# Optimization experiments

Measured on AMD Instinct MI355X. Metric: run time of the kernel, lower is better.

The kernel has to match this reference:

```python
import jax, jax.numpy as jnp
import numpy as np

# Dimensions
T = 1024      # tokens
D = 1024      # d_model
DFF = 1024    # expert intermediate dim
R = 64        # tucker rank (r_in == r_out)
G = 8         # n_group
E = 32        # experts_per_group
NEXP = G * E  # 256 routed experts
K = 8         # top-k


def setup_inputs() -> dict:
    key = jax.random.key(0)
    ks = jax.random.split(key, 12)
    s = 0.02
    return {
        "x": jax.random.normal(ks[0], (T, D), jnp.float32),
        "Wg": jax.random.normal(ks[1], (D, NEXP), jnp.float32) * s,
        "uin_gate": jax.random.normal(ks[2], (G, D, R), jnp.float32) * s,
        "core_gate": jax.random.normal(ks[3], (G, E, R, R), jnp.float32) * s,
        "uout_gate": jax.random.normal(ks[4], (G, R, DFF), jnp.float32) * s,
        "uin_up": jax.random.normal(ks[5], (G, D, R), jnp.float32) * s,
        "core_up": jax.random.normal(ks[6], (G, E, R, R), jnp.float32) * s,
        "uout_up": jax.random.normal(ks[7], (G, R, DFF), jnp.float32) * s,
        "uin_down": jax.random.normal(ks[8], (G, DFF, R), jnp.float32) * s,
        "core_down": jax.random.normal(ks[9], (G, E, R, R), jnp.float32) * s,
        "uout_down": jax.random.normal(ks[10], (G, R, D), jnp.float32) * s,
    }


def _moe_forward(x, Wg, uin_gate, core_gate, uout_gate,
                 uin_up, core_up, uout_up,
                 uin_down, core_down, uout_down):
    Tn, d = x.shape
    # Router: top-k over 256 experts, softmax over the k logits (fp32 as in torch)
    logits = x @ Wg                                   # [T, NEXP]
    w, sel = jax.lax.top_k(logits, K)                 # [T, K]
    w = jax.nn.softmax(w.astype(jnp.float32), axis=-1).astype(x.dtype)

    e = sel.reshape(-1)                               # [F] global expert id
    g = e // E                                        # [F] group id
    tok = jnp.repeat(jnp.arange(Tn), K)               # [F] source token id
    mask = (g[:, None] == jnp.arange(G)[None, :]).astype(x.dtype)  # [F, G]

    def gather_in(uin):
        # project tokens with every group's u_in once, then gather per pair
        pre = jnp.einsum('td,gdr->gtr', x, uin)       # [G, T, R]
        return pre[g, tok]                            # [F, R]

    def core_apply(xin, core):
        # per-pair Tucker core slice bmm: x.unsqueeze(1) @ core[rel_idx]
        slices = core.reshape(G * E, R, R)[e]         # [F, R, R] gather
        return jnp.einsum('fr,fro->fo', xin, slices)  # [F, R]

    def group_out(h, U):
        # per-pair group-specific projection: h[f] @ U[g_f]
        out = jnp.zeros((h.shape[0], U.shape[-1]), h.dtype)
        for gi in range(G):  # fixed small loop over 8 groups
            out = out + (h * mask[:, gi:gi + 1]) @ U[gi]
        return out

    gate_h = group_out(core_apply(gather_in(uin_gate), core_gate), uout_gate)  # [F, DFF]
    up_h = group_out(core_apply(gather_in(uin_up), core_up), uout_up)          # [F, DFF]
    act = jax.nn.silu(gate_h) * up_h                                           # SwiGLU
    xin_d = group_out(act, uin_down)                                           # [F, R]
    out_f = group_out(core_apply(xin_d, core_down), uout_down)                 # [F, D]
    out_f = out_f * w.reshape(-1)[:, None]
    # scatter-add expert outputs back to tokens
    return jax.ops.segment_sum(out_f, tok, num_segments=Tn)


def reference(x, Wg, uin_gate, core_gate, uout_gate,
              uin_up, core_up, uout_up,
              uin_down, core_down, uout_down):
    return _moe_forward(x, Wg, uin_gate, core_gate, uout_gate,
                        uin_up, core_up, uout_up,
                        uin_down, core_down, uout_down)
```

## Files before the change

kernel.cpp:

```cpp
#include <hip/hip_runtime.h>
#include <hip/hip_bf16.h>
#include <math.h>


#define T_ 1024
#define D_ 1024
#define DFF_ 1024
#define R_ 64
#define G_ 8
#define E_ 32
#define NEXP_ 256
#define K_ 8
#define F_ 8192
#define LKZ_ 4
#define LTB_ 8
#define PKZ_ 2
#define DKZ_ 4
#define LP_ 72

typedef short bf16x8 __attribute__((ext_vector_type(8)));
typedef float f32x4 __attribute__((ext_vector_type(4)));

__device__ __forceinline__ unsigned short f2bf(float f) {
  unsigned int u = __float_as_uint(f);
  u += 0x7fffu + ((u >> 16) & 1u);
  return (unsigned short)(u >> 16);
}

__device__ __forceinline__ void stage_tile(short* dst, const unsigned short* src,
                                           int gp, int tid) {
  for (int idx = tid; idx < 512; idx += 256) {
    int r = idx >> 3, c8 = (idx & 7) << 3;
    *(uint4*)&dst[r * LP_ + c8] = *(const uint4*)&src[(size_t)r * gp + c8];
  }
}

__device__ __forceinline__ void stage_tile_guard(short* dst, const unsigned short* src,
                                                 int gp, int rows_valid, int tid) {
  for (int idx = tid; idx < 512; idx += 256) {
    int r = idx >> 3, c8 = (idx & 7) << 3;
    uint4 v = make_uint4(0u, 0u, 0u, 0u);
    if (r < rows_valid) v = *(const uint4*)&src[(size_t)r * gp + c8];
    *(uint4*)&dst[r * LP_ + c8] = v;
  }
}

__device__ __forceinline__ void stage_tile_f32(short* dst, const float* src,
                                               int gp, int tid) {
  for (int idx = tid; idx < 512; idx += 256) {
    int r = idx >> 3, c8 = (idx & 7) << 3;
    const float* s = &src[(size_t)r * gp + c8];
    float4 v0 = *(const float4*)s;
    float4 v1 = *(const float4*)(s + 4);
    uint4 u;
    u.x = ((unsigned)f2bf(v0.y) << 16) | f2bf(v0.x);
    u.y = ((unsigned)f2bf(v0.w) << 16) | f2bf(v0.z);
    u.z = ((unsigned)f2bf(v1.y) << 16) | f2bf(v1.x);
    u.w = ((unsigned)f2bf(v1.w) << 16) | f2bf(v1.z);
    *(uint4*)&dst[r * LP_ + c8] = u;
  }
}

__device__ __forceinline__ void mma_strip(const short* As, const short* Bs,
                                          int ms, int lane, f32x4* acc) {
  int lm = lane & 15;
  int lk = (lane >> 4) << 3;
#pragma unroll
  for (int kc = 0; kc < 64; kc += 32) {
    bf16x8 a = *(const bf16x8*)&As[(ms + lm) * LP_ + kc + lk];
#pragma unroll
    for (int nt = 0; nt < 4; ++nt) {
      bf16x8 b = *(const bf16x8*)&Bs[(nt * 16 + lm) * LP_ + kc + lk];
      acc[nt] = __builtin_amdgcn_mfma_f32_16x16x32_bf16(a, b, acc[nt], 0, 0, 0);
    }
  }
}

__global__ __launch_bounds__(256) void k_prep_logits(
    const float* __restrict__ x, const float* __restrict__ Wg,
    const float* __restrict__ s0, const float* __restrict__ s1,
    const float* __restrict__ s2, const float* __restrict__ s3,
    const float* __restrict__ s4, const float* __restrict__ s5,
    unsigned short* __restrict__ xb,
    unsigned short* __restrict__ d0, unsigned short* __restrict__ d1,
    unsigned short* __restrict__ d2, unsigned short* __restrict__ d3,
    unsigned short* __restrict__ d4, unsigned short* __restrict__ d5,
    int* __restrict__ cnt, float* __restrict__ Yf, float* __restrict__ lp) {
  __shared__ float shbuf[64 * 65];
  int b = blockIdx.x;
  if (b < 896) {
    int id = b >> 7, rem = b & 127, g = rem >> 4, tile = rem & 15;
    if (id == 6) {
      size_t base = ((size_t)g * 16 + tile) * 8192;
      for (int i = threadIdx.x; i < 2048; i += 256) {
        size_t idx = base + (size_t)i * 4;
        float4 v = *(const float4*)&x[idx];
        xb[idx + 0] = f2bf(v.x);
        xb[idx + 1] = f2bf(v.y);
        xb[idx + 2] = f2bf(v.z);
        xb[idx + 3] = f2bf(v.w);
      }
      size_t ybase = ((size_t)g * 16 + tile) * 4096;
      float4 z4 = make_float4(0.f, 0.f, 0.f, 0.f);
      for (int i = threadIdx.x; i < 1024; i += 256)
        *(float4*)&Yf[ybase + (size_t)i * 4] = z4;
      if (g == 0 && tile == 0) cnt[threadIdx.x] = 0;
      return;
    }
    const float* src = id == 0 ? s0 : id == 1 ? s1 : id == 2 ? s2 : id == 3 ? s3 : id == 4 ? s4 : s5;
    unsigned short* dst = id == 0 ? d0 : id == 1 ? d1 : id == 2 ? d2 : id == 3 ? d3 : id == 4 ? d4 : d5;
    if (id < 3) {
      int r0 = tile * 64;
      for (int idx = threadIdx.x; idx < 4096; idx += 256) {
        int r = idx >> 6, c = idx & 63;
        shbuf[r * 65 + c] = src[((size_t)g * 1024 + r0 + r) * 64 + c];
      }
      __syncthreads();
      for (int idx = threadIdx.x; idx < 4096; idx += 256) {
        int c = idx >> 6, r = idx & 63;
        dst[((size_t)g * 64 + c) * 1024 + r0 + r] = f2bf(shbuf[r * 65 + c]);
      }
    } else {
      int c0 = tile * 64;
      for (int idx = threadIdx.x; idx < 4096; idx += 256) {
        int r = idx >> 6, c = idx & 63;
        shbuf[r * 65 + c] = src[((size_t)g * 64 + r) * 1024 + c0 + c];
      }
      __syncthreads();
      if (id == 5) {
        for (int idx = threadIdx.x; idx < 4096; idx += 256) {
          int c = idx >> 6, r = idx & 63;
          dst[(size_t)(c0 + c) * 512 + g * 64 + r] = f2bf(shbuf[r * 65 + c]);
        }
      } else {
        for (int idx = threadIdx.x; idx < 4096; idx += 256) {
          int c = idx >> 6, r = idx & 63;
          dst[((size_t)g * 1024 + c0 + c) * 64 + r] = f2bf(shbuf[r * 65 + c]);
        }
      }
    }
    return;
  }
  int lb = b - 896;
  int t0 = (lb & 127) * LTB_;
  int z = lb >> 7;
  int e = threadIdx.x;
  float* xs = shbuf;
  float a[LTB_] = {};
  int dc = z * 256;
  {
    int idx = threadIdx.x * 8;
    int tl = idx >> 8, d = idx & 255;
    *(float4*)&xs[tl * 256 + d] = *(const float4*)&x[(size_t)(t0 + tl) * D_ + dc + d];
    *(float4*)&xs[tl * 256 + d + 4] = *(const float4*)&x[(size_t)(t0 + tl) * D_ + dc + d + 4];
  }
  __syncthreads();
#pragma unroll 2
  for (int d2 = 0; d2 < 256; d2 += 4) {
    float w0 = Wg[(size_t)(dc + d2 + 0) * NEXP_ + e];
    float w1 = Wg[(size_t)(dc + d2 + 1) * NEXP_ + e];
    float w2 = Wg[(size_t)(dc + d2 + 2) * NEXP_ + e];
    float w3 = Wg[(size_t)(dc + d2 + 3) * NEXP_ + e];
#pragma unroll
    for (int j = 0; j < LTB_; ++j) {
      float4 xv = *(const float4*)&xs[j * 256 + d2];
      float aj = a[j];
      aj = fmaf(xv.x, w0, aj);
      aj = fmaf(xv.y, w1, aj);
      aj = fmaf(xv.z, w2, aj);
      aj = fmaf(xv.w, w3, aj);
      a[j] = aj;
    }
  }
  size_t base = (size_t)z * T_ * NEXP_;
#pragma unroll
  for (int j = 0; j < LTB_; ++j)
    lp[base + (size_t)(t0 + j) * NEXP_ + e] = a[j];
}

__global__ __launch_bounds__(256) void k_pre_topk(
    const unsigned short* __restrict__ xb,
    const unsigned short* __restrict__ uinT_g, const unsigned short* __restrict__ uinT_u,
    const float* __restrict__ lp,
    float* __restrict__ Pgp, float* __restrict__ Pup,
    float* __restrict__ wsm, int* __restrict__ bucket, int* __restrict__ cnt) {
  __shared__ short sh2[2 * 64 * LP_];
  int b = blockIdx.x;
  if (b < 512) {
    int tile = b & 15, g = (b >> 4) & 7, zz = b >> 7;
    int gu = zz >> 1, kz = zz & 1;
    const unsigned short* U = gu ? uinT_u : uinT_g;
    float* P = gu ? Pup : Pgp;
    int t0 = tile * 64;
    short* As = sh2;
    short* Bs = sh2 + 64 * LP_;
    int tid = threadIdx.x, lane = tid & 63, ms = (tid >> 6) * 16;
    f32x4 acc[4] = {};
    int dlo = kz * (D_ / PKZ_);
    for (int dc = dlo; dc < dlo + D_ / PKZ_; dc += 64) {
      stage_tile(As, xb + (size_t)t0 * D_ + dc, D_, tid);
      stage_tile(Bs, U + (size_t)g * 64 * 1024 + dc, 1024, tid);
      __syncthreads();
      mma_strip(As, Bs, ms, lane, acc);
      __syncthreads();
    }
    int lm = lane & 15, lq = (lane >> 4) * 4;
#pragma unroll
    for (int nt = 0; nt < 4; ++nt)
#pragma unroll
      for (int r = 0; r < 4; ++r)
        P[((size_t)(kz * G_ + g) * T_ + t0 + ms + lq + r) * R_ + nt * 16 + lm] = acc[nt][r];
    return;
  }
  int tb = b - 512;
  int wave = threadIdx.x >> 6;
  int lane = threadIdx.x & 63;
  int t = tb * 4 + wave;
  float v[4];
  int idx[4];
#pragma unroll
  for (int j = 0; j < 4; ++j) {
    idx[j] = lane + 64 * j;
    float s = 0.f;
#pragma unroll
    for (int z = 0; z < LKZ_; ++z)
      s += lp[(size_t)z * T_ * NEXP_ + (size_t)t * NEXP_ + idx[j]];
    v[j] = s;
  }
  float topv[K_];
  int topi[K_];
#pragma unroll
  for (int k = 0; k < K_; ++k) {
    float bv = v[0];
    int bi = idx[0];
#pragma unroll
    for (int j = 1; j < 4; ++j)
      if (v[j] > bv || (v[j] == bv && idx[j] < bi)) { bv = v[j]; bi = idx[j]; }
#pragma unroll
    for (int off = 32; off > 0; off >>= 1) {
      float ov = __shfl_xor(bv, off);
      int oi = __shfl_xor(bi, off);
      if (ov > bv || (ov == bv && oi < bi)) { bv = ov; bi = oi; }
    }
    topv[k] = bv;
    topi[k] = bi;
#pragma unroll
    for (int j = 0; j < 4; ++j)
      if (idx[j] == bi) v[j] = -INFINITY;
  }
  float m = topv[0];
  float ev[K_];
  float s = 0.f;
#pragma unroll
  for (int k = 0; k < K_; ++k) { ev[k] = expf(topv[k] - m); s += ev[k]; }
  float inv = 1.f / s;
  if (lane < K_) {
    wsm[t * K_ + lane] = ev[lane] * inv;
    int r1 = atomicAdd(&cnt[topi[lane]], 1);
    bucket[topi[lane] * 1024 + r1] = t * K_ + lane;
  }
}

__global__ __launch_bounds__(256) void k_scan(const int* __restrict__ cnt,
                                              int* __restrict__ off) {
  __shared__ int s[NEXP_];
  int i = threadIdx.x;
  s[i] = cnt[i];
  __syncthreads();
  for (int d = 1; d < NEXP_; d <<= 1) {
    int v = (i >= d) ? s[i - d] : 0;
    __syncthreads();
    s[i] += v;
    __syncthreads();
  }
  off[i + 1] = s[i];
  if (i == 0) off[0] = 0;
}

__global__ __launch_bounds__(256) void k_core_gu(const float* __restrict__ Pgp,
                                                 const float* __restrict__ Pup,
                                                 const float* __restrict__ core_g,
                                                 const float* __restrict__ core_u,
                                                 const int* __restrict__ bucket,
                                                 const int* __restrict__ off,
                                                 unsigned short* __restrict__ xgb,
                                                 unsigned short* __restrict__ xub) {
  int e = blockIdx.x >> 1, half = blockIdx.x & 1;
  int g = e >> 5;
  __shared__ float cg[4096], cu[4096];
  __shared__ float rg[4][64], ru[4][64];
  int tid = threadIdx.x;
  for (int i = tid; i < 1024; i += 256) {
    *(float4*)&cg[i * 4] = *(const float4*)&core_g[(size_t)e * 4096 + (size_t)i * 4];
    *(float4*)&cu[i * 4] = *(const float4*)&core_u[(size_t)e * 4096 + (size_t)i * 4];
  }
  int p0 = off[e], n = off[e + 1] - p0;
  int hn = (n + 1) >> 1;
  int i0 = half * hn;
  int i1 = i0 + hn; if (i1 > n) i1 = n;
  int pl = tid >> 6, o = tid & 63;
  __syncthreads();
  for (int ib = i0; ib < i1; ib += 4) {
    int i = ib + pl;
    bool valid = i < i1;
    int p = p0 + i;
    float sg = 0.f, su = 0.f;
    if (valid) {
      int t = bucket[e * 1024 + i] >> 3;
#pragma unroll
      for (int kz = 0; kz < PKZ_; ++kz) {
        sg += Pgp[((size_t)(kz * G_ + g) * T_ + t) * R_ + o];
        su += Pup[((size_t)(kz * G_ + g) * T_ + t) * R_ + o];
      }
    }
    __syncthreads();
    rg[pl][o] = sg;
    ru[pl][o] = su;
    __syncthreads();
    if (valid) {
      float ag = 0.f, au = 0.f;
#pragma unroll 8
      for (int r = 0; r < R_; ++r) {
        ag = fmaf(rg[pl][r], cg[r * R_ + o], ag);
        au = fmaf(ru[pl][r], cu[r * R_ + o], au);
      }
      xgb[(size_t)p * R_ + o] = f2bf(ag);
      xub[(size_t)p * R_ + o] = f2bf(au);
    }
  }
}

__global__ __launch_bounds__(256) void k_fused_ad(const unsigned short* __restrict__ xgb,
                                                  const unsigned short* __restrict__ xub,
                                                  const unsigned short* __restrict__ uoutT_g,
                                                  const unsigned short* __restrict__ uoutT_u,
                                                  const unsigned short* __restrict__ uinT_d,
                                                  const int* __restrict__ off,
                                                  float* __restrict__ xdp) {
  int g = blockIdx.y;
  int kz = blockIdx.z;
  int p0 = off[g * E_];
  int pend = off[g * E_ + E_];
  int ntiles = (pend - p0 + 63) >> 6;
  __shared__ short Ag[64 * LP_], Au[64 * LP_];
  __shared__ short Bg[64 * LP_], Bu[64 * LP_], Bd[64 * LP_];
  __shared__ short Pt[64 * LP_];
  int tid = threadIdx.x, lane = tid & 63, ms = (tid >> 6) * 16;
  int lm = lane & 15, lq = (lane >> 4) * 4;
  for (int tile = blockIdx.x; tile < ntiles; tile += gridDim.x) {
    int pbase = p0 + tile * 64;
    int rv = pend - pbase; if (rv > 64) rv = 64;
    stage_tile_guard(Ag, xgb + (size_t)pbase * R_, R_, rv, tid);
    stage_tile_guard(Au, xub + (size_t)pbase * R_, R_, rv, tid);
    f32x4 accd[4] = {};
#pragma unroll
    for (int c4 = 0; c4 < 4; ++c4) {
      int cc = kz * (DFF_ / DKZ_) + c4 * 64;
      stage_tile(Bg, uoutT_g + ((size_t)g * DFF_ + cc) * R_, R_, tid);
      stage_tile(Bu, uoutT_u + ((size_t)g * DFF_ + cc) * R_, R_, tid);
      stage_tile(Bd, uinT_d + (size_t)g * 64 * 1024 + cc, 1024, tid);
      __syncthreads();
      f32x4 accg[4] = {}, accu[4] = {};
      mma_strip(Ag, Bg, ms, lane, accg);
      mma_strip(Au, Bu, ms, lane, accu);
#pragma unroll
      for (int nt = 0; nt < 4; ++nt)
#pragma unroll
        for (int r = 0; r < 4; ++r) {
          float gv = accg[nt][r];
          float av = gv / (1.f + expf(-gv)) * accu[nt][r];
          Pt[(ms + lq + r) * LP_ + nt * 16 + lm] = (short)f2bf(av);
        }
      mma_strip(Pt, Bd, ms, lane, accd);
      __syncthreads();
    }
#pragma unroll
    for (int nt = 0; nt < 4; ++nt)
#pragma unroll
      for (int r = 0; r < 4; ++r) {
        int p = pbase + ms + lq + r;
        if (p < pend) xdp[((size_t)kz * F_ + p) * R_ + nt * 16 + lm] = accd[nt][r];
      }
    __syncthreads();
  }
}

__global__ __launch_bounds__(256) void k_down_core(const float* __restrict__ xdp,
                                                   const float* __restrict__ core_d,
                                                   const int* __restrict__ bucket,
                                                   const float* __restrict__ wsm,
                                                   const int* __restrict__ off,
                                                   float* __restrict__ Yf) {
  int e = blockIdx.x >> 1, half = blockIdx.x & 1;
  int g = e >> 5;
  __shared__ float cd[4096];
  __shared__ float xs[4][64];
  int tid = threadIdx.x;
  for (int i = tid; i < 1024; i += 256)
    *(float4*)&cd[i * 4] = *(const float4*)&core_d[(size_t)e * 4096 + (size_t)i * 4];
  int p0 = off[e], n = off[e + 1] - p0;
  int hn = (n + 1) >> 1;
  int i0 = half * hn;
  int i1 = i0 + hn; if (i1 > n) i1 = n;
  int pl = tid >> 6, o = tid & 63;
  __syncthreads();
  for (int ib = i0; ib < i1; ib += 4) {
    int i = ib + pl;
    bool valid = i < i1;
    int p = p0 + i;
    int f = valid ? bucket[e * 1024 + i] : 0;
    float s = 0.f;
    if (valid) {
#pragma unroll
      for (int kz = 0; kz < DKZ_; ++kz) s += xdp[((size_t)kz * F_ + p) * R_ + o];
    }
    __syncthreads();
    xs[pl][o] = s;
    __syncthreads();
    if (valid) {
      float a = 0.f;
#pragma unroll 8
      for (int r = 0; r < R_; ++r) a = fmaf(xs[pl][r], cd[r * R_ + o], a);
      atomicAdd(&Yf[(size_t)(f >> 3) * 512 + g * 64 + o], wsm[f] * a);
    }
  }
}

__global__ __launch_bounds__(256) void k_fin(const float* __restrict__ Yf,
                                             const unsigned short* __restrict__ Uod2T,
                                             float* __restrict__ out) {
  int t0 = blockIdx.x * 64;
  int d0 = blockIdx.y * 64;
  __shared__ short As[64 * LP_], Bs[64 * LP_];
  __shared__ float Os[64 * 68];
  int tid = threadIdx.x, lane = tid & 63, ms = (tid >> 6) * 16;
  int lm = lane & 15, lq = (lane >> 4) * 4;
  f32x4 acc[4] = {};
  for (int kc = 0; kc < 512; kc += 64) {
    stage_tile_f32(As, Yf + (size_t)t0 * 512 + kc, 512, tid);
    stage_tile(Bs, Uod2T + (size_t)d0 * 512 + kc, 512, tid);
    __syncthreads();
    mma_strip(As, Bs, ms, lane, acc);
    __syncthreads();
  }
#pragma unroll
  for (int nt = 0; nt < 4; ++nt)
#pragma unroll
    for (int r = 0; r < 4; ++r)
      Os[(ms + lq + r) * 68 + nt * 16 + lm] = acc[nt][r];
  __syncthreads();
  for (int idx = tid; idx < 1024; idx += 256) {
    int r = idx >> 4, c4 = (idx & 15) << 2;
    *(float4*)&out[(size_t)(t0 + r) * D_ + d0 + c4] = *(const float4*)&Os[r * 68 + c4];
  }
}

extern "C" void kernel_launch(void* const* d_in, const int* in_sizes, int n_in,
                              void* d_out, int out_size, void* d_ws, size_t ws_size,
                              hipStream_t stream) {
  const float* x = (const float*)d_in[0];
  const float* Wg = (const float*)d_in[1];
  const float* uin_gate = (const float*)d_in[2];
  const float* core_gate = (const float*)d_in[3];
  const float* uout_gate = (const float*)d_in[4];
  const float* uin_up = (const float*)d_in[5];
  const float* core_up = (const float*)d_in[6];
  const float* uout_up = (const float*)d_in[7];
  const float* uin_down = (const float*)d_in[8];
  const float* core_down = (const float*)d_in[9];
  const float* uout_down = (const float*)d_in[10];
  float* out = (float*)d_out;

  char* ws = (char*)d_ws;
  size_t o = 0;
  auto alloc = [&](size_t bytes) { size_t r = o; o = (o + bytes + 255) & ~(size_t)255; return r; };
  size_t o_lp = alloc((size_t)LKZ_ * T_ * NEXP_ * 4);
  size_t o_wsm = alloc(F_ * 4);
  size_t o_bucket = alloc((size_t)NEXP_ * 1024 * 4);
  size_t o_cnt = alloc(NEXP_ * 4);
  size_t o_off = alloc((NEXP_ + 1) * 4);
  size_t o_xb = alloc((size_t)T_ * D_ * 2);
  size_t o_uinT_g = alloc((size_t)G_ * 64 * 1024 * 2);
  size_t o_uinT_u = alloc((size_t)G_ * 64 * 1024 * 2);
  size_t o_uinT_d = alloc((size_t)G_ * 64 * 1024 * 2);
  size_t o_uoutT_g = alloc((size_t)G_ * 1024 * 64 * 2);
  size_t o_uoutT_u = alloc((size_t)G_ * 1024 * 64 * 2);
  size_t o_Uod2T = alloc((size_t)D_ * 512 * 2);
  size_t o_xgb = alloc((size_t)F_ * R_ * 2);
  size_t o_xub = alloc((size_t)F_ * R_ * 2);
  size_t o_Y = alloc((size_t)T_ * 512 * 4);
  size_t o_pgp = alloc((size_t)PKZ_ * G_ * T_ * R_ * 4);
  size_t o_pup = alloc((size_t)PKZ_ * G_ * T_ * R_ * 4);
  size_t o_xdp = alloc((size_t)DKZ_ * F_ * R_ * 4);
  (void)ws_size;

  float* lp = (float*)(ws + o_lp);
  float* wsm = (float*)(ws + o_wsm);
  int* bucket = (int*)(ws + o_bucket);
  int* cnt = (int*)(ws + o_cnt);
  int* off = (int*)(ws + o_off);
  unsigned short* xb = (unsigned short*)(ws + o_xb);
  unsigned short* uinT_g = (unsigned short*)(ws + o_uinT_g);
  unsigned short* uinT_u = (unsigned short*)(ws + o_uinT_u);
  unsigned short* uinT_d = (unsigned short*)(ws + o_uinT_d);
  unsigned short* uoutT_g = (unsigned short*)(ws + o_uoutT_g);
  unsigned short* uoutT_u = (unsigned short*)(ws + o_uoutT_u);
  unsigned short* Uod2T = (unsigned short*)(ws + o_Uod2T);
  unsigned short* xgb = (unsigned short*)(ws + o_xgb);
  unsigned short* xub = (unsigned short*)(ws + o_xub);
  float* Yf = (float*)(ws + o_Y);
  float* pgp = (float*)(ws + o_pgp);
  float* pup = (float*)(ws + o_pup);
  float* xdp = (float*)(ws + o_xdp);

  k_prep_logits<<<1408, 256, 0, stream>>>(x, Wg, uin_gate, uin_up, uin_down,
                                          uout_gate, uout_up, uout_down, xb,
                                          uinT_g, uinT_u, uinT_d,
                                          uoutT_g, uoutT_u, Uod2T, cnt, Yf, lp);
  k_pre_topk<<<768, 256, 0, stream>>>(xb, uinT_g, uinT_u, lp, pgp, pup, wsm, bucket, cnt);
  k_scan<<<1, 256, 0, stream>>>(cnt, off);
  k_core_gu<<<NEXP_ * 2, 256, 0, stream>>>(pgp, pup, core_gate, core_up, bucket, off, xgb, xub);
  k_fused_ad<<<dim3(16, G_, DKZ_), 256, 0, stream>>>(xgb, xub, uoutT_g, uoutT_u, uinT_d, off, xdp);
  k_down_core<<<NEXP_ * 2, 256, 0, stream>>>(xdp, core_down, bucket, wsm, off, Yf);
  k_fin<<<dim3(16, 16), 256, 0, stream>>>(Yf, Uod2T, out);
}
```

Measured before the change: 208.5 us.

## Fuse router logits, top-k and scan into the projection kernel with last-block ticket

```diff
diff --git a/kernel.cpp b/kernel.cpp
--- a/kernel.cpp
+++ b/kernel.cpp
@@ -12,8 +12,6 @@
 #define NEXP_ 256
 #define K_ 8
 #define F_ 8192
-#define LKZ_ 4
-#define LTB_ 8
 #define PKZ_ 2
 #define DKZ_ 4
 #define LP_ 72
@@ -76,8 +74,8 @@
   }
 }
 
-__global__ __launch_bounds__(256) void k_prep_logits(
-    const float* __restrict__ x, const float* __restrict__ Wg,
+__global__ __launch_bounds__(256) void k_prep(
+    const float* __restrict__ x,
     const float* __restrict__ s0, const float* __restrict__ s1,
     const float* __restrict__ s2, const float* __restrict__ s3,
     const float* __restrict__ s4, const float* __restrict__ s5,
@@ -85,116 +83,85 @@
     unsigned short* __restrict__ d0, unsigned short* __restrict__ d1,
     unsigned short* __restrict__ d2, unsigned short* __restrict__ d3,
     unsigned short* __restrict__ d4, unsigned short* __restrict__ d5,
-    int* __restrict__ cnt, float* __restrict__ Yf, float* __restrict__ lp) {
+    int* __restrict__ cnt, int* __restrict__ tickets, float* __restrict__ Yf) {
   __shared__ float shbuf[64 * 65];
   int b = blockIdx.x;
-  if (b < 896) {
-    int id = b >> 7, rem = b & 127, g = rem >> 4, tile = rem & 15;
-    if (id == 6) {
-      size_t base = ((size_t)g * 16 + tile) * 8192;
-      for (int i = threadIdx.x; i < 2048; i += 256) {
-        size_t idx = base + (size_t)i * 4;
-        float4 v = *(const float4*)&x[idx];
-        xb[idx + 0] = f2bf(v.x);
-        xb[idx + 1] = f2bf(v.y);
-        xb[idx + 2] = f2bf(v.z);
-        xb[idx + 3] = f2bf(v.w);
-      }
-      size_t ybase = ((size_t)g * 16 + tile) * 4096;
-      float4 z4 = make_float4(0.f, 0.f, 0.f, 0.f);
-      for (int i = threadIdx.x; i < 1024; i += 256)
-        *(float4*)&Yf[ybase + (size_t)i * 4] = z4;
-      if (g == 0 && tile == 0) cnt[threadIdx.x] = 0;
-      return;
-    }
-    const float* src = id == 0 ? s0 : id == 1 ? s1 : id == 2 ? s2 : id == 3 ? s3 : id == 4 ? s4 : s5;
-    unsigned short* dst = id == 0 ? d0 : id == 1 ? d1 : id == 2 ? d2 : id == 3 ? d3 : id == 4 ? d4 : d5;
-    if (id < 3) {
-      int r0 = tile * 64;
-      for (int idx = threadIdx.x; idx < 4096; idx += 256) {
-        int r = idx >> 6, c = idx & 63;
-        shbuf[r * 65 + c] = src[((size_t)g * 1024 + r0 + r) * 64 + c];
-      }
-      __syncthreads();
+  int id = b >> 7, rem = b & 127, g = rem >> 4, tile = rem & 15;
+  if (id == 6) {
+    size_t base = ((size_t)g * 16 + tile) * 8192;
+    for (int i = threadIdx.x; i < 2048; i += 256) {
+      size_t idx = base + (size_t)i * 4;
+      float4 v = *(const float4*)&x[idx];
+      xb[idx + 0] = f2bf(v.x);
+      xb[idx + 1] = f2bf(v.y);
+      xb[idx + 2] = f2bf(v.z);
+      xb[idx + 3] = f2bf(v.w);
+    }
+    size_t ybase = ((size_t)g * 16 + tile) * 4096;
+    float4 z4 = make_float4(0.f, 0.f, 0.f, 0.f);
+    for (int i = threadIdx.x; i < 1024; i += 256)
+      *(float4*)&Yf[ybase + (size_t)i * 4] = z4;
+    if (g == 0 && tile == 0) {
+      cnt[threadIdx.x] = 0;
+      if (threadIdx.x == 0) tickets[0] = 0;
+    }
+    return;
+  }
+  const float* src = id == 0 ? s0 : id == 1 ? s1 : id == 2 ? s2 : id == 3 ? s3 : id == 4 ? s4 : s5;
+  unsigned short* dst = id == 0 ? d0 : id == 1 ? d1 : id == 2 ? d2 : id == 3 ? d3 : id == 4 ? d4 : d5;
+  if (id < 3) {
+    int r0 = tile * 64;
+    for (int idx = threadIdx.x; idx < 4096; idx += 256) {
+      int r = idx >> 6, c = idx & 63;
+      shbuf[r * 65 + c] = src[((size_t)g * 1024 + r0 + r) * 64 + c];
+    }
+    __syncthreads();
+    for (int idx = threadIdx.x; idx < 4096; idx += 256) {
+      int c = idx >> 6, r = idx & 63;
+      dst[((size_t)g * 64 + c) * 1024 + r0 + r] = f2bf(shbuf[r * 65 + c]);
+    }
+  } else {
+    int c0 = tile * 64;
+    for (int idx = threadIdx.x; idx < 4096; idx += 256) {
+      int r = idx >> 6, c = idx & 63;
+      shbuf[r * 65 + c] = src[((size_t)g * 64 + r) * 1024 + c0 + c];
+    }
+    __syncthreads();
+    if (id == 5) {
       for (int idx = threadIdx.x; idx < 4096; idx += 256) {
         int c = idx >> 6, r = idx & 63;
-        dst[((size_t)g * 64 + c) * 1024 + r0 + r] = f2bf(shbuf[r * 65 + c]);
+        dst[(size_t)(c0 + c) * 512 + g * 64 + r] = f2bf(shbuf[r * 65 + c]);
       }
     } else {
-      int c0 = tile * 64;
       for (int idx = threadIdx.x; idx < 4096; idx += 256) {
-        int r = idx >> 6, c = idx & 63;
-        shbuf[r * 65 + c] = src[((size_t)g * 64 + r) * 1024 + c0 + c];
+        int c = idx >> 6, r = idx & 63;
+        dst[((size_t)g * 1024 + c0 + c) * 64 + r] = f2bf(shbuf[r * 65 + c]);
       }
-      __syncthreads();
-      if (id == 5) {
-        for (int idx = threadIdx.x; idx < 4096; idx += 256) {
-          int c = idx >> 6, r = idx & 63;
-          dst[(size_t)(c0 + c) * 512 + g * 64 + r] = f2bf(shbuf[r * 65 + c]);
-        }
-      } else {
-        for (int idx = threadIdx.x; idx < 4096; idx += 256) {
-          int c = idx >> 6, r = idx & 63;
-          dst[((size_t)g * 1024 + c0 + c) * 64 + r] = f2bf(shbuf[r * 65 + c]);
-        }
-      }
-    }
-    return;
-  }
-  int lb = b - 896;
-  int t0 = (lb & 127) * LTB_;
-  int z = lb >> 7;
-  int e = threadIdx.x;
-  float* xs = shbuf;
-  float a[LTB_] = {};
-  int dc = z * 256;
-  {
-    int idx = threadIdx.x * 8;
-    int tl = idx >> 8, d = idx & 255;
-    *(float4*)&xs[tl * 256 + d] = *(const float4*)&x[(size_t)(t0 + tl) * D_ + dc + d];
-    *(float4*)&xs[tl * 256 + d + 4] = *(const float4*)&x[(size_t)(t0 + tl) * D_ + dc + d + 4];
-  }
-  __syncthreads();
-#pragma unroll 2
-  for (int d2 = 0; d2 < 256; d2 += 4) {
-    float w0 = Wg[(size_t)(dc + d2 + 0) * NEXP_ + e];
-    float w1 = Wg[(size_t)(dc + d2 + 1) * NEXP_ + e];
-    float w2 = Wg[(size_t)(dc + d2 + 2) * NEXP_ + e];
-    float w3 = Wg[(size_t)(dc + d2 + 3) * NEXP_ + e];
-#pragma unroll
-    for (int j = 0; j < LTB_; ++j) {
-      float4 xv = *(const float4*)&xs[j * 256 + d2];
-      float aj = a[j];
-      aj = fmaf(xv.x, w0, aj);
-      aj = fmaf(xv.y, w1, aj);
-      aj = fmaf(xv.z, w2, aj);
-      aj = fmaf(xv.w, w3, aj);
-      a[j] = aj;
-    }
-  }
-  size_t base = (size_t)z * T_ * NEXP_;
-#pragma unroll
-  for (int j = 0; j < LTB_; ++j)
-    lp[base + (size_t)(t0 + j) * NEXP_ + e] = a[j];
-}
-
-__global__ __launch_bounds__(256) void k_pre_topk(
+    }
+  }
+}
+
+__global__ __launch_bounds__(256) void k_pre_router(
+    const float* __restrict__ x, const float* __restrict__ Wg,
     const unsigned short* __restrict__ xb,
     const unsigned short* __restrict__ uinT_g, const unsigned short* __restrict__ uinT_u,
-    const float* __restrict__ lp,
     float* __restrict__ Pgp, float* __restrict__ Pup,
-    float* __restrict__ wsm, int* __restrict__ bucket, int* __restrict__ cnt) {
-  __shared__ short sh2[2 * 64 * LP_];
+    float* __restrict__ wsm, int* __restrict__ bucket, int* __restrict__ cnt,
+    int* __restrict__ tickets, int* __restrict__ off) {
+  __shared__ float smf[8192];
+  __shared__ int lastfl;
   int b = blockIdx.x;
-  if (b < 512) {
-    int tile = b & 15, g = (b >> 4) & 7, zz = b >> 7;
+  int tid = threadIdx.x;
+  if (b >= 128) {
+    int b2 = b - 128;
+    int tile = b2 & 15, g = (b2 >> 4) & 7, zz = b2 >> 7;
     int gu = zz >> 1, kz = zz & 1;
     const unsigned short* U = gu ? uinT_u : uinT_g;
     float* P = gu ? Pup : Pgp;
     int t0 = tile * 64;
-    short* As = sh2;
-    short* Bs = sh2 + 64 * LP_;
-    int tid = threadIdx.x, lane = tid & 63, ms = (tid >> 6) * 16;
+    short* As = (short*)smf;
+    short* Bs = (short*)smf + 64 * LP_;
+    int lane = tid & 63, ms = (tid >> 6) * 16;
     f32x4 acc[4] = {};
     int dlo = kz * (D_ / PKZ_);
     for (int dc = dlo; dc < dlo + D_ / PKZ_; dc += 64) {
@@ -212,69 +179,99 @@
         P[((size_t)(kz * G_ + g) * T_ + t0 + ms + lq + r) * R_ + nt * 16 + lm] = acc[nt][r];
     return;
   }
-  int tb = b - 512;
-  int wave = threadIdx.x >> 6;
-  int lane = threadIdx.x & 63;
-  int t = tb * 4 + wave;
-  float v[4];
-  int idx[4];
-#pragma unroll
-  for (int j = 0; j < 4; ++j) {
-    idx[j] = lane + 64 * j;
+  int t0 = b * 8;
+  for (int i = tid; i < 2048; i += 256) {
+    int j = i >> 8, d4 = (i & 255) << 2;
+    *(float4*)&smf[j * 1024 + d4] = *(const float4*)&x[(size_t)(t0 + j) * D_ + d4];
+  }
+  __syncthreads();
+  int e = tid;
+  float a[8] = {};
+#pragma unroll 2
+  for (int d2 = 0; d2 < 1024; d2 += 4) {
+    float w0 = Wg[(size_t)(d2 + 0) * NEXP_ + e];
+    float w1 = Wg[(size_t)(d2 + 1) * NEXP_ + e];
+    float w2 = Wg[(size_t)(d2 + 2) * NEXP_ + e];
+    float w3 = Wg[(size_t)(d2 + 3) * NEXP_ + e];
+#pragma unroll
+    for (int j = 0; j < 8; ++j) {
+      float4 xv = *(const float4*)&smf[j * 1024 + d2];
+      float aj = a[j];
+      aj = fmaf(xv.x, w0, aj);
+      aj = fmaf(xv.y, w1, aj);
+      aj = fmaf(xv.z, w2, aj);
+      aj = fmaf(xv.w, w3, aj);
+      a[j] = aj;
+    }
+  }
+  __syncthreads();
+  float* lg = smf;
+#pragma unroll
+  for (int j = 0; j < 8; ++j) lg[j * 256 + e] = a[j];
+  __syncthreads();
+  int wave = tid >> 6, lane = tid & 63;
+  for (int kk = 0; kk < 2; ++kk) {
+    int j = wave * 2 + kk;
+    int t = t0 + j;
+    float v[4];
+    int idx[4];
+#pragma unroll
+    for (int j2 = 0; j2 < 4; ++j2) {
+      idx[j2] = lane + 64 * j2;
+      v[j2] = lg[j * 256 + idx[j2]];
+    }
+    float topv[K_];
+    int topi[K_];
+#pragma unroll
+    for (int k = 0; k < K_; ++k) {
+      float bv = v[0];
+      int bi = idx[0];
+#pragma unroll
+      for (int j2 = 1; j2 < 4; ++j2)
+        if (v[j2] > bv || (v[j2] == bv && idx[j2] < bi)) { bv = v[j2]; bi = idx[j2]; }
+#pragma unroll
+      for (int o2 = 32; o2 > 0; o2 >>= 1) {
+        float ov = __shfl_xor(bv, o2);
+        int oi = __shfl_xor(bi, o2);
+        if (ov > bv || (ov == bv && oi < bi)) { bv = ov; bi = oi; }
+      }
+      topv[k] = bv;
+      topi[k] = bi;
+#pragma unroll
+      for (int j2 = 0; j2 < 4; ++j2)
+        if (idx[j2] == bi) v[j2] = -INFINITY;
+    }
+    float m = topv[0];
+    float ev[K_];
     float s = 0.f;
 #pragma unroll
-    for (int z = 0; z < LKZ_; ++z)
-      s += lp[(size_t)z * T_ * NEXP_ + (size_t)t * NEXP_ + idx[j]];
-    v[j] = s;
-  }
-  float topv[K_];
-  int topi[K_];
-#pragma unroll
-  for (int k = 0; k < K_; ++k) {
-    float bv = v[0];
-    int bi = idx[0];
-#pragma unroll
-    for (int j = 1; j < 4; ++j)
-      if (v[j] > bv || (v[j] == bv && idx[j] < bi)) { bv = v[j]; bi = idx[j]; }
-#pragma unroll
-    for (int off = 32; off > 0; off >>= 1) {
-      float ov = __shfl_xor(bv, off);
-      int oi = __shfl_xor(bi, off);
-      if (ov > bv || (ov == bv && oi < bi)) { bv = ov; bi = oi; }
-    }
-    topv[k] = bv;
-    topi[k] = bi;
-#pragma unroll
-    for (int j = 0; j < 4; ++j)
-      if (idx[j] == bi) v[j] = -INFINITY;
-  }
-  float m = topv[0];
-  float ev[K_];
-  float s = 0.f;
-#pragma unroll
-  for (int k = 0; k < K_; ++k) { ev[k] = expf(topv[k] - m); s += ev[k]; }
-  float inv = 1.f / s;
-  if (lane < K_) {
-    wsm[t * K_ + lane] = ev[lane] * inv;
-    int r1 = atomicAdd(&cnt[topi[lane]], 1);
-    bucket[topi[lane] * 1024 + r1] = t * K_ + lane;
-  }
-}
-
-__global__ __launch_bounds__(256) void k_scan(const int* __restrict__ cnt,
-                                              int* __restrict__ off) {
-  __shared__ int s[NEXP_];
-  int i = threadIdx.x;
-  s[i] = cnt[i];
-  __syncthreads();
-  for (int d = 1; d < NEXP_; d <<= 1) {
-    int v = (i >= d) ? s[i - d] : 0;
-    __syncthreads();
-    s[i] += v;
-    __syncthreads();
-  }
-  off[i + 1] = s[i];
-  if (i == 0) off[0] = 0;
+    for (int k = 0; k < K_; ++k) { ev[k] = expf(topv[k] - m); s += ev[k]; }
+    float inv = 1.f / s;
+    if (lane < K_) {
+      wsm[t * K_ + lane] = ev[lane] * inv;
+      int r1 = atomicAdd(&cnt[topi[lane]], 1);
+      bucket[topi[lane] * 1024 + r1] = t * K_ + lane;
+    }
+  }
+  __threadfence();
+  __syncthreads();
+  if (tid == 0) lastfl = (atomicAdd(&tickets[0], 1) == 127) ? 1 : 0;
+  __syncthreads();
+  if (lastfl) {
+    int* s = (int*)smf;
+    int i = tid;
+    int c0 = atomicAdd(&cnt[i], 0);
+    s[i] = c0;
+    __syncthreads();
+    for (int d = 1; d < NEXP_; d <<= 1) {
+      int vv = (i >= d) ? s[i - d] : 0;
+      __syncthreads();
+      s[i] += vv;
+      __syncthreads();
+    }
+    off[i + 1] = s[i];
+    if (i == 0) off[0] = 0;
+  }
 }
 
 __global__ __launch_bounds__(256) void k_core_gu(const float* __restrict__ Pgp,
@@ -474,10 +471,10 @@
   char* ws = (char*)d_ws;
   size_t o = 0;
   auto alloc = [&](size_t bytes) { size_t r = o; o = (o + bytes + 255) & ~(size_t)255; return r; };
-  size_t o_lp = alloc((size_t)LKZ_ * T_ * NEXP_ * 4);
   size_t o_wsm = alloc(F_ * 4);
   size_t o_bucket = alloc((size_t)NEXP_ * 1024 * 4);
   size_t o_cnt = alloc(NEXP_ * 4);
+  size_t o_tickets = alloc(256);
   size_t o_off = alloc((NEXP_ + 1) * 4);
   size_t o_xb = alloc((size_t)T_ * D_ * 2);
   size_t o_uinT_g = alloc((size_t)G_ * 64 * 1024 * 2);
@@ -494,10 +491,10 @@
   size_t o_xdp = alloc((size_t)DKZ_ * F_ * R_ * 4);
   (void)ws_size;
 
-  float* lp = (float*)(ws + o_lp);
   float* wsm = (float*)(ws + o_wsm);
   int* bucket = (int*)(ws + o_bucket);
   int* cnt = (int*)(ws + o_cnt);
+  int* tickets = (int*)(ws + o_tickets);
   int* off = (int*)(ws + o_off);
   unsigned short* xb = (unsigned short*)(ws + o_xb);
   unsigned short* uinT_g = (unsigned short*)(ws + o_uinT_g);
@@ -513,12 +510,12 @@
   float* pup = (float*)(ws + o_pup);
   float* xdp = (float*)(ws + o_xdp);
 
-  k_prep_logits<<<1408, 256, 0, stream>>>(x, Wg, uin_gate, uin_up, uin_down,
-                                          uout_gate, uout_up, uout_down, xb,
-                                          uinT_g, uinT_u, uinT_d,
-                                          uoutT_g, uoutT_u, Uod2T, cnt, Yf, lp);
-  k_pre_topk<<<768, 256, 0, stream>>>(xb, uinT_g, uinT_u, lp, pgp, pup, wsm, bucket, cnt);
-  k_scan<<<1, 256, 0, stream>>>(cnt, off);
+  k_prep<<<896, 256, 0, stream>>>(x, uin_gate, uin_up, uin_down,
+                                  uout_gate, uout_up, uout_down, xb,
+                                  uinT_g, uinT_u, uinT_d,
+                                  uoutT_g, uoutT_u, Uod2T, cnt, tickets, Yf);
+  k_pre_router<<<640, 256, 0, stream>>>(x, Wg, xb, uinT_g, uinT_u,
+                                        pgp, pup, wsm, bucket, cnt, tickets, off);
   k_core_gu<<<NEXP_ * 2, 256, 0, stream>>>(pgp, pup, core_gate, core_up, bucket, off, xgb, xub);
   k_fused_ad<<<dim3(16, G_, DKZ_), 256, 0, stream>>>(xgb, xub, uoutT_g, uoutT_u, uinT_d, off, xdp);
   k_down_core<<<NEXP_ * 2, 256, 0, stream>>>(xdp, core_down, bucket, wsm, off, Yf);
```

Result: slower. 239.6 us (+14.9%).
